# Optimization experiments

Hardware: AMD Instinct MI355X
Metric: run time of the kernel (lower is better)

## Reference

```python
import jax, jax.numpy as jnp
import numpy as np

NUM_HEADS = 32
NUM_KV_HEADS = 8
HEAD_DIM = 128
NEG_INF = -1e9


def rotate_half(x):
    x1, x2 = jnp.split(x, 2, axis=-1)
    return jnp.concatenate([-x2, x1], axis=-1)


def setup_inputs() -> dict:
    key = jax.random.key(0)
    ks = jax.random.split(key, 8)
    B, S, H = 2, 2048, 4096
    hidden_states = jax.random.normal(ks[0], (B, S, H), jnp.float32) * 0.02
    # additive causal mask [1,1,S,S]: 0 on/below diagonal, -1e9 above
    causal = jnp.tril(jnp.ones((S, S), bool))
    attention_mask = jnp.where(causal, 0.0, NEG_INF)[None, None, :, :].astype(jnp.float32)
    # RoPE tables (theta=500000 style), shape [1,S,head_dim]
    inv_freq = 1.0 / (500000.0 ** (np.arange(0, HEAD_DIM, 2, dtype=np.float32) / HEAD_DIM))
    t = np.arange(S, dtype=np.float32)
    freqs = np.outer(t, inv_freq)  # [S, head_dim/2]
    emb = np.concatenate([freqs, freqs], axis=-1)  # [S, head_dim]
    cos = jnp.asarray(np.cos(emb))[None]
    sin = jnp.asarray(np.sin(emb))[None]
    scale = 0.02
    wq = jax.random.normal(ks[1], (NUM_HEADS * HEAD_DIM, H), jnp.float32) * scale
    wk = jax.random.normal(ks[2], (NUM_KV_HEADS * HEAD_DIM, H), jnp.float32) * scale
    wv = jax.random.normal(ks[3], (NUM_KV_HEADS * HEAD_DIM, H), jnp.float32) * scale
    wo = jax.random.normal(ks[4], (H, NUM_HEADS * HEAD_DIM), jnp.float32) * scale
    return {"hidden_states": hidden_states, "attention_mask": attention_mask,
            "cos": cos, "sin": sin, "wq": wq, "wk": wk, "wv": wv, "wo": wo}


def reference(hidden_states, attention_mask, cos, sin, wq, wk, wv, wo):
    B, S, H = hidden_states.shape
    nh, nkv, hd = NUM_HEADS, NUM_KV_HEADS, HEAD_DIM
    groups = nh // nkv
    # QKV projections (bias=False)
    q = jnp.einsum('bsh,dh->bsd', hidden_states, wq).reshape(B, S, nh, hd).transpose(0, 2, 1, 3)
    k = jnp.einsum('bsh,dh->bsd', hidden_states, wk).reshape(B, S, nkv, hd).transpose(0, 2, 1, 3)
    v = jnp.einsum('bsh,dh->bsd', hidden_states, wv).reshape(B, S, nkv, hd).transpose(0, 2, 1, 3)
    # RoPE: cos/sin [1,S,hd] -> broadcast over head dim [1,1,S,hd]
    c = cos[:, None, :, :]
    s = sin[:, None, :, :]
    q = q * c + rotate_half(q) * s
    k = k * c + rotate_half(k) * s
    # GQA: repeat_kv
    k = jnp.repeat(k, groups, axis=1)  # [B,nh,S,hd]
    v = jnp.repeat(v, groups, axis=1)
    # SDPA with additive mask
    scores = jnp.einsum('bhqd,bhkd->bhqk', q, k) / jnp.sqrt(jnp.float32(hd))
    scores = scores + attention_mask[:, :, :, :k.shape[2]]
    attn = jax.nn.softmax(scores, axis=-1)
    out = jnp.einsum('bhqk,bhkd->bhqd', attn, v)  # [B,nh,S,hd]
    out = out.transpose(0, 2, 1, 3).reshape(B, S, nh * hd)
    return jnp.einsum('bsd,hd->bsh', out, wo)
```

## Files before the change

kernel.cpp:

```cpp
#include <hip/hip_runtime.h>
#include <hip/hip_bf16.h>

typedef __attribute__((ext_vector_type(8))) __bf16 bf16x8;
typedef __attribute__((ext_vector_type(4))) float f32x4;
typedef __attribute__((ext_vector_type(16))) float f32x16;
typedef __attribute__((ext_vector_type(4))) unsigned int u32x4;

#define SEQ 2048
#define NH 32
#define NKV 8
#define HD 128

__device__ __forceinline__ ushort f2bf(float f) {
  unsigned u = __builtin_bit_cast(unsigned, f);
  unsigned r = (u + 0x7fffu + ((u >> 16) & 1u)) >> 16;
  return (ushort)r;
}
__device__ __forceinline__ float bf2f(ushort h) {
  return __builtin_bit_cast(float, ((unsigned)h) << 16);
}
__device__ __forceinline__ unsigned cvt_pk_bf16(float lo, float hi) {
  unsigned r;
  asm("v_cvt_pk_bf16_f32 %0, %1, %2" : "=v"(r) : "v"(lo), "v"(hi));
  return r;
}
__device__ __forceinline__ float exp2_fast(float x) {
  float r;
  asm("v_exp_f32 %0, %1" : "=v"(r) : "v"(x));
  return r;
}
__device__ __forceinline__ void gload16(const void* g, void* l) {
  __builtin_amdgcn_global_load_lds(
      (const __attribute__((address_space(1))) void*)g,
      (__attribute__((address_space(3))) void*)l, 16, 0, 0);
}

__global__ __launch_bounds__(256) void f2bf_kernel(const float4* __restrict__ in,
                                                   ushort4* __restrict__ out, int n4) {
  int i = blockIdx.x * 256 + threadIdx.x;
  if (i >= n4) return;
  float4 v = in[i];
  ushort4 o;
  o.x = f2bf(v.x); o.y = f2bf(v.y); o.z = f2bf(v.z); o.w = f2bf(v.w);
  out[i] = o;
}

template <int OUTF32>
__global__ __launch_bounds__(256) void gemm_bt_kernel(const ushort* __restrict__ A,
                                                      const ushort* __restrict__ B,
                                                      void* __restrict__ C,
                                                      int M, int N, int K) {
  __shared__ ushort As[2][128 * 32];
  __shared__ ushort Bs[2][128 * 32];
  const int tid = threadIdx.x;
  const int w = tid >> 6, l = tid & 63;
  const int lr = l & 15, lc = l >> 4;
  const int bx = blockIdx.x, by = blockIdx.y;
  const int wr = w >> 1, wc = w & 1;

  f32x4 z = {0.f, 0.f, 0.f, 0.f};
  f32x4 acc[4][4];
#pragma unroll
  for (int i = 0; i < 4; ++i)
#pragma unroll
    for (int j = 0; j < 4; ++j) acc[i][j] = z;

  const ushort* aSrc = A + (size_t)(by * 128 + 32 * w + (l >> 2)) * K + (l & 3) * 8;
  const ushort* bSrc = B + (size_t)(bx * 128 + 32 * w + (l >> 2)) * K + (l & 3) * 8;
  const int ldsOff = (32 * w) * 32;

#pragma unroll
  for (int q = 0; q < 2; ++q) {
    gload16(aSrc + (size_t)q * 16 * K, &As[0][ldsOff + q * 512]);
    gload16(bSrc + (size_t)q * 16 * K, &Bs[0][ldsOff + q * 512]);
  }
  __syncthreads();

  const int nk = K >> 5;
  int cur = 0;
  for (int kt = 0; kt < nk; ++kt) {
    if (kt + 1 < nk) {
      const ushort* a2 = aSrc + (size_t)(kt + 1) * 32;
      const ushort* b2 = bSrc + (size_t)(kt + 1) * 32;
#pragma unroll
      for (int q = 0; q < 2; ++q) {
        gload16(a2 + (size_t)q * 16 * K, &As[cur ^ 1][ldsOff + q * 512]);
        gload16(b2 + (size_t)q * 16 * K, &Bs[cur ^ 1][ldsOff + q * 512]);
      }
    }
    bf16x8 af[4], bfr[4];
#pragma unroll
    for (int i = 0; i < 4; ++i)
      af[i] = *(const bf16x8*)&As[cur][(64 * wr + 16 * i + lr) * 32 + lc * 8];
#pragma unroll
    for (int j = 0; j < 4; ++j)
      bfr[j] = *(const bf16x8*)&Bs[cur][(64 * wc + 16 * j + lr) * 32 + lc * 8];
#pragma unroll
    for (int i = 0; i < 4; ++i)
#pragma unroll
      for (int j = 0; j < 4; ++j)
        acc[i][j] = __builtin_amdgcn_mfma_f32_16x16x32_bf16(af[i], bfr[j], acc[i][j], 0, 0, 0);
    __syncthreads();
    cur ^= 1;
  }

#pragma unroll
  for (int i = 0; i < 4; ++i)
#pragma unroll
    for (int j = 0; j < 4; ++j) {
      int row = by * 128 + 64 * wr + 16 * i + lc * 4;
      int col = bx * 128 + 64 * wc + 16 * j + lr;
#pragma unroll
      for (int r = 0; r < 4; ++r) {
        if (OUTF32)
          ((float*)C)[(size_t)(row + r) * N + col] = acc[i][j][r];
        else
          ((ushort*)C)[(size_t)(row + r) * N + col] = f2bf(acc[i][j][r]);
      }
    }
}

template <int OUTF32>
__global__ __launch_bounds__(512, 2) void gemm256_kernel(const ushort* __restrict__ A,
                                                         const ushort* __restrict__ B,
                                                         void* __restrict__ C,
                                                         int M, int N, int K) {
  __shared__ ushort As[2][256 * 64];
  __shared__ ushort Bs[2][256 * 64];
  const int tid = threadIdx.x;
  const int w = tid >> 6, l = tid & 63;
  const int lr = l & 15, lc = l >> 4;
  const int wr = w >> 2, wc = w & 3;

  const int nbx = N >> 8;
  const int cpx = gridDim.x >> 3;
  const int sw = (blockIdx.x & 7) * cpx + (blockIdx.x >> 3);
  const int bx = sw % nbx, by = sw / nbx;

  const ushort* Asrc = A + (size_t)(by * 256) * K;
  const ushort* Bsrc = B + (size_t)(bx * 256) * K;

  f32x4 z = {0.f, 0.f, 0.f, 0.f};
  f32x4 acc[8][4];
#pragma unroll
  for (int m = 0; m < 8; ++m)
#pragma unroll
    for (int n = 0; n < 4; ++n) acc[m][n] = z;

  const int NK = K >> 6;

  auto stage = [&](int kt2, int s) {
    if (kt2 >= NK) return;
    const int mat = s >> 1, half = s & 1;
    const ushort* g = mat ? Bsrc : Asrc;
    char* lb = (char*)(mat ? &Bs[kt2 & 1][0] : &As[kt2 & 1][0]) + half * 16384 + w * 1024;
#pragma unroll
    for (int i = 0; i < 2; ++i) {
      int row = half * 128 + i * 64 + w * 8 + (l >> 3);
      int csw = ((l & 7) * 16) ^ ((row & 7) << 4);
      gload16(g + (size_t)row * K + kt2 * 64 + (csw >> 1), lb + i * 8192);
    }
  };

  stage(0, 0); stage(0, 1); stage(0, 2); stage(0, 3);
  stage(1, 0);

  bf16x8 af[4][2], bfr[4][2];
  for (int kt = 0; kt < NK; ++kt) {
    const char* Ab = (const char*)&As[kt & 1][0];
    const char* Bb = (const char*)&Bs[kt & 1][0];
    if (kt + 1 < NK) asm volatile("s_waitcnt vmcnt(2)" ::: "memory");
    else             asm volatile("s_waitcnt vmcnt(0)" ::: "memory");
    asm volatile("s_barrier" ::: "memory");

#pragma unroll
    for (int m = 0; m < 4; ++m) {
      int row = wr * 128 + m * 16 + lr;
#pragma unroll
      for (int ks = 0; ks < 2; ++ks)
        af[m][ks] = *(const bf16x8*)(Ab + row * 128 + ((ks * 64 + lc * 16) ^ ((row & 7) << 4)));
    }
#pragma unroll
    for (int n = 0; n < 2; ++n) {
      int row = wc * 64 + n * 16 + lr;
#pragma unroll
      for (int ks = 0; ks < 2; ++ks)
        bfr[n][ks] = *(const bf16x8*)(Bb + row * 128 + ((ks * 64 + lc * 16) ^ ((row & 7) << 4)));
    }
    stage(kt + 1, 1);
    __builtin_amdgcn_s_setprio(1);
#pragma unroll
    for (int m = 0; m < 4; ++m)
#pragma unroll
      for (int n = 0; n < 2; ++n)
#pragma unroll
        for (int ks = 0; ks < 2; ++ks)
          acc[m][n] = __builtin_amdgcn_mfma_f32_16x16x32_bf16(af[m][ks], bfr[n][ks], acc[m][n], 0, 0, 0);
    __builtin_amdgcn_s_setprio(0);
    asm volatile("s_barrier" ::: "memory");

#pragma unroll
    for (int n = 2; n < 4; ++n) {
      int row = wc * 64 + n * 16 + lr;
#pragma unroll
      for (int ks = 0; ks < 2; ++ks)
        bfr[n][ks] = *(const bf16x8*)(Bb + row * 128 + ((ks * 64 + lc * 16) ^ ((row & 7) << 4)));
    }
    stage(kt + 1, 2);
    __builtin_amdgcn_s_setprio(1);
#pragma unroll
    for (int m = 0; m < 4; ++m)
#pragma unroll
      for (int n = 2; n < 4; ++n)
#pragma unroll
        for (int ks = 0; ks < 2; ++ks)
          acc[m][n] = __builtin_amdgcn_mfma_f32_16x16x32_bf16(af[m][ks], bfr[n][ks], acc[m][n], 0, 0, 0);
    __builtin_amdgcn_s_setprio(0);
    asm volatile("s_barrier" ::: "memory");

#pragma unroll
    for (int m = 0; m < 4; ++m) {
      int row = wr * 128 + (m + 4) * 16 + lr;
#pragma unroll
      for (int ks = 0; ks < 2; ++ks)
        af[m][ks] = *(const bf16x8*)(Ab + row * 128 + ((ks * 64 + lc * 16) ^ ((row & 7) << 4)));
    }
    stage(kt + 1, 3);
    __builtin_amdgcn_s_setprio(1);
#pragma unroll
    for (int m = 0; m < 4; ++m)
#pragma unroll
      for (int n = 0; n < 2; ++n)
#pragma unroll
        for (int ks = 0; ks < 2; ++ks)
          acc[m + 4][n] = __builtin_amdgcn_mfma_f32_16x16x32_bf16(af[m][ks], bfr[n][ks], acc[m + 4][n], 0, 0, 0);
    __builtin_amdgcn_s_setprio(0);
    asm volatile("s_barrier" ::: "memory");

    stage(kt + 2, 0);
    __builtin_amdgcn_s_setprio(1);
#pragma unroll
    for (int m = 0; m < 4; ++m)
#pragma unroll
      for (int n = 2; n < 4; ++n)
#pragma unroll
        for (int ks = 0; ks < 2; ++ks)
          acc[m + 4][n] = __builtin_amdgcn_mfma_f32_16x16x32_bf16(af[m][ks], bfr[n][ks], acc[m + 4][n], 0, 0, 0);
    __builtin_amdgcn_s_setprio(0);
  }

#pragma unroll
  for (int m = 0; m < 8; ++m)
#pragma unroll
    for (int n = 0; n < 4; ++n) {
      int row = by * 256 + wr * 128 + m * 16 + lc * 4;
      int col = bx * 256 + wc * 64 + n * 16 + lr;
#pragma unroll
      for (int r = 0; r < 4; ++r) {
        if (OUTF32)
          ((float*)C)[(size_t)(row + r) * N + col] = acc[m][n][r];
        else
          ((ushort*)C)[(size_t)(row + r) * N + col] = f2bf(acc[m][n][r]);
      }
    }
}

__global__ __launch_bounds__(256) void rope_kernel(const ushort* __restrict__ in, int ld,
                                                   const float* __restrict__ cosb,
                                                   const float* __restrict__ sinb,
                                                   ushort* __restrict__ out,
                                                   int hshift, float scale) {
  int idx = blockIdx.x * 256 + threadIdx.x;
  int d = idx & 63;
  int nh = 1 << hshift;
  int h = (idx >> 6) & (nh - 1);
  int rowg = idx >> (6 + hshift);
  int s = rowg & (SEQ - 1);
  int b = rowg >> 11;
  const ushort* p = in + (size_t)rowg * ld + h * HD + d;
  float x = bf2f(p[0]), y = bf2f(p[64]);
  float c = cosb[s * HD + d], sn = sinb[s * HD + d];
  ushort* qo = out + (((size_t)(b * nh + h)) * SEQ + s) * HD + d;
  qo[0] = f2bf((x * c - y * sn) * scale);
  qo[64] = f2bf((y * c + x * sn) * scale);
}

__global__ __launch_bounds__(256) void vtrans_kernel(const ushort* __restrict__ vin,
                                                     ushort* __restrict__ vout) {
  __shared__ ushort t[64][66];
  const int s0 = blockIdx.x * 64;
  const int c0 = blockIdx.y * 64;
  const int b = blockIdx.z;
  const int tx = threadIdx.x & 63;
  const int ty = threadIdx.x >> 6;
#pragma unroll
  for (int rr = 0; rr < 64; rr += 4) {
    int r = rr + ty;
    t[r][tx] = vin[((size_t)(b * SEQ + s0 + r)) * 2048 + 1024 + c0 + tx];
  }
  __syncthreads();
#pragma unroll
  for (int rr = 0; rr < 64; rr += 4) {
    int c = rr + ty;
    int cg = c0 + c;
    int kvh = cg >> 7, d = cg & 127;
    vout[(((size_t)(b * NKV + kvh)) * HD + d) * SEQ + s0 + tx] = t[tx][c];
  }
}

__global__ __launch_bounds__(256, 2) void attn_kernel(const ushort* __restrict__ Qh,
                                                      const ushort* __restrict__ Kh,
                                                      const ushort* __restrict__ Vt,
                                                      ushort* __restrict__ Out) {
  __shared__ ushort Kl[2][64 * 128];

  const int tid = threadIdx.x;
  const int w = tid >> 6, l = tid & 63;
  const int lq = l & 31;
  const int hl = l >> 5;

  const int n = blockIdx.x;
  const int xcd = n & 7, i = n >> 3;
  const int a = i & 7;
  const int r = i >> 3;
  const int r0 = r & 3, sl = r >> 2;
  const int qt = (sl == 0) ? r0 : (sl == 1) ? (7 - r0) : (sl == 2) ? (8 + r0) : (15 - r0);
  const int pp = 2 * xcd + (a >> 2);
  const int h2 = a & 3;
  const int bb = pp >> 3, kvh = pp & 7;
  const int hh = kvh * 4 + h2;
  const int bh = bb * 32 + hh;
  const int q0 = qt * 128;
  const int wrow0 = q0 + 32 * w;
  const int qrow = wrow0 + lq;

  const ushort* Kbase = Kh + ((size_t)(bb * NKV + kvh) * SEQ) * HD;
  const ushort* Vbase = Vt + ((size_t)(bb * NKV + kvh) * HD) * SEQ;

  bf16x8 qf[8];
  {
    const ushort* qrp = Qh + ((size_t)bh * SEQ + qrow) * HD + 8 * hl;
#pragma unroll
    for (int s8 = 0; s8 < 8; ++s8) qf[s8] = *(const bf16x8*)(qrp + 16 * s8);
  }

  f32x16 o[4];
#pragma unroll
  for (int db = 0; db < 4; ++db)
#pragma unroll
    for (int i2 = 0; i2 < 16; ++i2) o[db][i2] = 0.f;
  float m_run = -1e30f, l_run = 0.f;

  const int ntw = 2 * qt + (w >> 1) + 1;
  const int ntb = 2 * qt + 2;

  auto stageK = [&](int buf, int t) {
    const int kv0 = t * 64;
#pragma unroll
    for (int q = 0; q < 4; ++q) {
      int chunk = 4 * w + q;
      int row = chunk * 4 + (l >> 4);
      int cs = ((l & 15) ^ (row & 7)) * 8;
      gload16(Kbase + ((size_t)(kv0 + row)) * HD + cs, &Kl[buf][chunk * 512]);
    }
  };

  stageK(0, 0);
  __syncthreads();

  int cur = 0;
  for (int t = 0; t < ntb; ++t) {
    const int kv0 = t * 64;
    if (t + 1 < ntb) stageK(cur ^ 1, t + 1);

    if (t < ntw) {
      f32x16 sacc[2];
#pragma unroll
      for (int b2 = 0; b2 < 2; ++b2)
#pragma unroll
        for (int i2 = 0; i2 < 16; ++i2) sacc[b2][i2] = 0.f;

      const int swz = lq & 7;
      __builtin_amdgcn_s_setprio(1);
#pragma unroll
      for (int s8 = 0; s8 < 8; ++s8) {
#pragma unroll
        for (int b2 = 0; b2 < 2; ++b2) {
          int row = 32 * b2 + lq;
          bf16x8 kf = *(const bf16x8*)((const char*)&Kl[cur][0] + row * 256 +
                                       (((2 * s8 + hl) ^ swz) << 4));
          sacc[b2] = __builtin_amdgcn_mfma_f32_32x32x16_bf16(kf, qf[s8], sacc[b2], 0, 0, 0);
        }
      }
      __builtin_amdgcn_s_setprio(0);

      if (t == ntw - 1) {
#pragma unroll
        for (int b2 = 0; b2 < 2; ++b2)
#pragma unroll
          for (int r2 = 0; r2 < 16; ++r2) {
            int kv = kv0 + 32 * b2 + (r2 & 3) + 8 * (r2 >> 2) + 4 * hl;
            if (kv > qrow) sacc[b2][r2] = -1e30f;
          }
      }

      float tm[8];
#pragma unroll
      for (int r2 = 0; r2 < 8; ++r2)
        tm[r2] = fmaxf(fmaxf(sacc[0][r2], sacc[0][r2 + 8]),
                       fmaxf(sacc[1][r2], sacc[1][r2 + 8]));
#pragma unroll
      for (int s2 = 4; s2; s2 >>= 1)
#pragma unroll
        for (int r2 = 0; r2 < s2; ++r2) tm[r2] = fmaxf(tm[r2], tm[r2 + s2]);
      float mx = fmaxf(tm[0], __shfl_xor(tm[0], 32));

      if (__any(mx > m_run + 8.0f)) {
        float mn = fmaxf(m_run, mx);
        float sc = exp2_fast(m_run - mn);
        m_run = mn;
        l_run *= sc;
#pragma unroll
        for (int db = 0; db < 4; ++db) o[db] *= sc;
      }

#pragma unroll
      for (int b2 = 0; b2 < 2; ++b2)
#pragma unroll
        for (int r2 = 0; r2 < 16; ++r2) sacc[b2][r2] = exp2_fast(sacc[b2][r2] - m_run);
      float ts[8];
#pragma unroll
      for (int r2 = 0; r2 < 8; ++r2)
        ts[r2] = (sacc[0][r2] + sacc[0][r2 + 8]) + (sacc[1][r2] + sacc[1][r2 + 8]);
#pragma unroll
      for (int s2 = 4; s2; s2 >>= 1)
#pragma unroll
        for (int r2 = 0; r2 < s2; ++r2) ts[r2] += ts[r2 + s2];
      l_run += ts[0] + __shfl_xor(ts[0], 32);

      unsigned pw[2][8];
#pragma unroll
      for (int b2 = 0; b2 < 2; ++b2)
#pragma unroll
        for (int i2 = 0; i2 < 8; ++i2)
          pw[b2][i2] = cvt_pk_bf16(sacc[b2][2 * i2], sacc[b2][2 * i2 + 1]);

#pragma unroll
      for (int s = 0; s < 4; ++s) {
        const int b2 = s >> 1, bs = 4 * (s & 1);
        unsigned wA = pw[b2][bs], wB = pw[b2][bs + 1], wC = pw[b2][bs + 2], wD = pw[b2][bs + 3];
        unsigned s1 = hl ? wA : wC, s2v = hl ? wB : wD;
        unsigned rx1 = (unsigned)__shfl_xor((int)s1, 32);
        unsigned rx2 = (unsigned)__shfl_xor((int)s2v, 32);
        u32x4 fw = {hl ? rx1 : wA, hl ? rx2 : wB, hl ? wC : rx1, hl ? wD : rx2};
        bf16x8 pfrag = __builtin_bit_cast(bf16x8, fw);
        const ushort* vp = Vbase + (size_t)lq * SEQ + kv0 + 16 * s + 8 * hl;
        bf16x8 vf[4];
#pragma unroll
        for (int db = 0; db < 4; ++db) vf[db] = *(const bf16x8*)(vp + (size_t)(32 * db) * SEQ);
        __builtin_amdgcn_s_setprio(1);
#pragma unroll
        for (int db = 0; db < 4; ++db)
          o[db] = __builtin_amdgcn_mfma_f32_32x32x16_bf16(vf[db], pfrag, o[db], 0, 0, 0);
        __builtin_amdgcn_s_setprio(0);
      }
    }
    __syncthreads();
    cur ^= 1;
  }

  const float inv = 1.0f / l_run;
  ushort* outp = Out + ((size_t)bb * SEQ + qrow) * (NH * HD) + hh * HD;
#pragma unroll
  for (int db = 0; db < 4; ++db)
#pragma unroll
    for (int i2 = 0; i2 < 8; ++i2) {
      unsigned wrd = cvt_pk_bf16(o[db][2 * i2] * inv, o[db][2 * i2 + 1] * inv);
      int d = 32 * db + 2 * (i2 & 1) + 8 * (i2 >> 1) + 4 * hl;
      *(unsigned*)(outp + d) = wrd;
    }
}

extern "C" void kernel_launch(void* const* d_in, const int* in_sizes, int n_in,
                              void* d_out, int out_size, void* d_ws, size_t ws_size,
                              hipStream_t stream) {
  const float* hs = (const float*)d_in[0];
  const float* cosb = (const float*)d_in[2];
  const float* sinb = (const float*)d_in[3];
  const float* wq = (const float*)d_in[4];
  const float* wk = (const float*)d_in[5];
  const float* wv = (const float*)d_in[6];
  const float* wo = (const float*)d_in[7];

  char* ws = (char*)d_ws;
  ushort* hs_bf = (ushort*)(ws);
  ushort* wq_bf = (ushort*)(ws + 33554432);
  ushort* wk_bf = (ushort*)(ws + 67108864);
  ushort* wv_bf = (ushort*)(ws + 75497472);
  ushort* wo_bf = (ushort*)(ws + 83886080);
  ushort* q_lin = (ushort*)(ws + 117440512);
  ushort* kv_lin = (ushort*)(ws + 150994944);
  ushort* Qh = hs_bf;
  ushort* Kh = wq_bf;
  ushort* Vt = (ushort*)(ws + 41943040);
  ushort* attn_out = q_lin;

  f2bf_kernel<<<16384, 256, 0, stream>>>((const float4*)hs, (ushort4*)hs_bf, 4194304);
  f2bf_kernel<<<16384, 256, 0, stream>>>((const float4*)wq, (ushort4*)wq_bf, 4194304);
  f2bf_kernel<<<4096, 256, 0, stream>>>((const float4*)wk, (ushort4*)wk_bf, 1048576);
  f2bf_kernel<<<4096, 256, 0, stream>>>((const float4*)wv, (ushort4*)wv_bf, 1048576);
  f2bf_kernel<<<16384, 256, 0, stream>>>((const float4*)wo, (ushort4*)wo_bf, 4194304);

  gemm256_kernel<0><<<256, 512, 0, stream>>>(hs_bf, wq_bf, q_lin, 4096, 4096, 4096);
  gemm_bt_kernel<0><<<dim3(16, 32), 256, 0, stream>>>(hs_bf, wk_bf, kv_lin, 4096, 2048, 4096);

  rope_kernel<<<32768, 256, 0, stream>>>(q_lin, 4096, cosb, sinb, Qh, 5,
                                         0.08838834764831845f * 1.4426950408889634f);
  rope_kernel<<<8192, 256, 0, stream>>>(kv_lin, 2048, cosb, sinb, Kh, 3, 1.0f);
  vtrans_kernel<<<dim3(32, 16, 2), 256, 0, stream>>>(kv_lin, Vt);

  attn_kernel<<<1024, 256, 0, stream>>>(Qh, Kh, Vt, attn_out);

  gemm256_kernel<1><<<256, 512, 0, stream>>>(attn_out, wo_bf, d_out, 4096, 4096, 4096);
}
```

Before: 571.1 us.

## Stage V tiles in LDS and pair complementary causal q-tiles per block

The attention block grows to 512 threads, with two 4-wave groups handling q-tiles qt and 15-qt of the same head. The pair's combined causal work is constant, so load across blocks evens out, and each staged K/V tile is shared by both groups. V tiles are now loaded cooperatively into swizzled shared memory alongside K, replacing per-lane strided global reads. In exchange LDS use per block doubles, and the group with the shorter tile idles at the barriers while the longer one finishes its extra iterations.

```diff
diff --git a/kernel.cpp b/kernel.cpp
--- a/kernel.cpp
+++ b/kernel.cpp
@@ -308,30 +308,31 @@
   }
 }
 
-__global__ __launch_bounds__(256, 2) void attn_kernel(const ushort* __restrict__ Qh,
+__global__ __launch_bounds__(512, 2) void attn_kernel(const ushort* __restrict__ Qh,
                                                       const ushort* __restrict__ Kh,
                                                       const ushort* __restrict__ Vt,
                                                       ushort* __restrict__ Out) {
   __shared__ ushort Kl[2][64 * 128];
+  __shared__ ushort Vl[2][128 * 64];
 
   const int tid = threadIdx.x;
   const int w = tid >> 6, l = tid & 63;
   const int lq = l & 31;
   const int hl = l >> 5;
+  const int g = w >> 2;
+  const int wl = w & 3;
 
   const int n = blockIdx.x;
   const int xcd = n & 7, i = n >> 3;
-  const int a = i & 7;
-  const int r = i >> 3;
-  const int r0 = r & 3, sl = r >> 2;
-  const int qt = (sl == 0) ? r0 : (sl == 1) ? (7 - r0) : (sl == 2) ? (8 + r0) : (15 - r0);
-  const int pp = 2 * xcd + (a >> 2);
-  const int h2 = a & 3;
+  const int qpi = i & 7;
+  const int h2 = (i >> 3) & 3;
+  const int pp = 2 * xcd + (i >> 5);
   const int bb = pp >> 3, kvh = pp & 7;
   const int hh = kvh * 4 + h2;
   const int bh = bb * 32 + hh;
+  const int qt = g ? (15 - qpi) : qpi;
   const int q0 = qt * 128;
-  const int wrow0 = q0 + 32 * w;
+  const int wrow0 = q0 + 32 * wl;
   const int qrow = wrow0 + lq;
 
   const ushort* Kbase = Kh + ((size_t)(bb * NKV + kvh) * SEQ) * HD;
@@ -351,27 +352,34 @@
     for (int i2 = 0; i2 < 16; ++i2) o[db][i2] = 0.f;
   float m_run = -1e30f, l_run = 0.f;
 
-  const int ntw = 2 * qt + (w >> 1) + 1;
-  const int ntb = 2 * qt + 2;
-
-  auto stageK = [&](int buf, int t) {
+  const int ntw = 2 * qt + (wl >> 1) + 1;
+  const int ntb = 2 * (15 - qpi) + 2;
+
+  auto stageKV = [&](int buf, int t) {
     const int kv0 = t * 64;
 #pragma unroll
-    for (int q = 0; q < 4; ++q) {
-      int chunk = 4 * w + q;
-      int row = chunk * 4 + (l >> 4);
+    for (int q = 0; q < 2; ++q) {
+      int c = 2 * w + q;
+      int row = c * 4 + (l >> 4);
       int cs = ((l & 15) ^ (row & 7)) * 8;
-      gload16(Kbase + ((size_t)(kv0 + row)) * HD + cs, &Kl[buf][chunk * 512]);
+      gload16(Kbase + ((size_t)(kv0 + row)) * HD + cs, &Kl[buf][c * 512]);
+    }
+#pragma unroll
+    for (int q = 0; q < 2; ++q) {
+      int c = 2 * w + q;
+      int row = c * 8 + (l >> 3);
+      int cs = ((l & 7) ^ (row & 7)) * 8;
+      gload16(Vbase + (size_t)row * SEQ + kv0 + cs, &Vl[buf][c * 512]);
     }
   };
 
-  stageK(0, 0);
+  stageKV(0, 0);
   __syncthreads();
 
   int cur = 0;
   for (int t = 0; t < ntb; ++t) {
     const int kv0 = t * 64;
-    if (t + 1 < ntb) stageK(cur ^ 1, t + 1);
+    if (t + 1 < ntb) stageKV(cur ^ 1, t + 1);
 
     if (t < ntw) {
       f32x16 sacc[2];
@@ -454,10 +462,13 @@
         unsigned rx2 = (unsigned)__shfl_xor((int)s2v, 32);
         u32x4 fw = {hl ? rx1 : wA, hl ? rx2 : wB, hl ? wC : rx1, hl ? wD : rx2};
         bf16x8 pfrag = __builtin_bit_cast(bf16x8, fw);
-        const ushort* vp = Vbase + (size_t)lq * SEQ + kv0 + 16 * s + 8 * hl;
         bf16x8 vf[4];
 #pragma unroll
-        for (int db = 0; db < 4; ++db) vf[db] = *(const bf16x8*)(vp + (size_t)(32 * db) * SEQ);
+        for (int db = 0; db < 4; ++db) {
+          int row = 32 * db + lq;
+          vf[db] = *(const bf16x8*)((const char*)&Vl[cur][0] + row * 128 +
+                                    (((2 * s + hl) ^ swz) << 4));
+        }
         __builtin_amdgcn_s_setprio(1);
 #pragma unroll
         for (int db = 0; db < 4; ++db)
@@ -519,7 +530,7 @@
   rope_kernel<<<8192, 256, 0, stream>>>(kv_lin, 2048, cosb, sinb, Kh, 3, 1.0f);
   vtrans_kernel<<<dim3(32, 16, 2), 256, 0, stream>>>(kv_lin, Vt);
 
-  attn_kernel<<<1024, 256, 0, stream>>>(Qh, Kh, Vt, attn_out);
+  attn_kernel<<<512, 512, 0, stream>>>(Qh, Kh, Vt, attn_out);
 
   gemm256_kernel<1><<<256, 512, 0, stream>>>(attn_out, wo_bf, d_out, 4096, 4096, 4096);
 }
```

Measured after the change: 535.9 us. -6.2%, faster.
